# Kernel optimization log

Hardware: AMD Instinct MI355X
Metric: run time of the kernel (lower is better)

Reference implementation:

```python
import jax, jax.numpy as jnp
import numpy as np

L, P = 16384, 512
DT_MIN, DT_MAX = 0.001, 0.1
THRESHOLD = 1.0  # spike threshold assumed for cartesian_spike


def setup_inputs() -> dict:
    key = jax.random.key(0)
    k1, k2, k3, k4, k5, k6 = jax.random.split(key, 6)
    u = jax.random.normal(k1, (L, P), dtype=jnp.float32)
    # Stored Lambda param: [..., 0] = log(-Re(Lambda)) with Re(Lambda) < 0, [..., 1] = Im(Lambda)
    lam_real_neg = jax.random.uniform(k2, (P,), minval=0.1, maxval=1.0)  # -Re(Lambda)
    lam_imag = jax.random.normal(k3, (P,)) * 3.0
    Lambda = jnp.stack([jnp.log(lam_real_neg), lam_imag], axis=-1).astype(jnp.float32)
    # init_log_steps: log(dt) uniform in [log(dt_min), log(dt_max)], shape (P, 1)
    log_step = (np.log(DT_MIN) + jax.random.uniform(k4, (P, 1)) * (np.log(DT_MAX) - np.log(DT_MIN))).astype(jnp.float32)
    V_re = jax.random.normal(k5, (P, P), dtype=jnp.float32) / np.sqrt(P)
    V_im = jax.random.normal(k6, (P, P), dtype=jnp.float32) / np.sqrt(P)
    return {"u": u, "Lambda": Lambda, "log_step": log_step, "V_re": V_re, "V_im": V_im}


def _binop(q_i, q_j):
    A_i, b_i = q_i
    A_j, b_j = q_j
    return (A_j * A_i, A_j * b_i + b_j)


def reference(u, Lambda, log_step, V_re, V_im):
    # keep_imag = False: u stays real. discretization = 'zoh', activation = 'cartesian_spike'.
    Lambda_tilde = -jnp.exp(Lambda[..., 0]) + 1j * Lambda[..., 1]            # (P,) complex
    step = jnp.exp(log_step[:, 0])                                            # (P,)
    Lambda_bar = jnp.exp(Lambda_tilde * step)                                 # (P,) |.|<1
    # B_tilde = I, so zoh gives B_bar = diag((Lambda_bar - 1)/Lambda); B_bar @ u_t = coef * u_t
    B_coef = (Lambda_bar - 1.0) / Lambda_tilde                                # (P,)
    Lambda_elements = jnp.broadcast_to(Lambda_bar, (u.shape[0], Lambda_bar.shape[0]))
    Bu_elements = B_coef[None, :] * u.astype(Lambda_bar.dtype)                # (L, P) complex
    _, xs = jax.lax.associative_scan(_binop, (Lambda_elements, Bu_elements))  # (L, P)
    V = V_re + 1j * V_im
    xs = xs @ V.T                                                             # vmap(V @ x) over L
    spikes = (xs.real > THRESHOLD).astype(jnp.float32)                        # cartesian_spike
    return spikes
```

## Files before the change

kernel.cpp:

```cpp
#include <hip/hip_runtime.h>

#define L_LEN   16384
#define P_DIM   512
#define CHUNK   128
#define NCHUNK  128

#define KDIM    1024
#define NDIM    512
#define BM      128
#define BN      128
#define BK      64

typedef __bf16 bf16_t;
typedef __bf16 bf16x8 __attribute__((ext_vector_type(8)));
typedef float  floatx4 __attribute__((ext_vector_type(4)));

__device__ __forceinline__ void channel_consts(const float* __restrict__ Lam,
                                               const float* __restrict__ lstep,
                                               int p, float& ar, float& ai,
                                               float& br, float& bi) {
    float lr = -expf(Lam[2 * p + 0]);
    float li = Lam[2 * p + 1];
    float s  = expf(lstep[p]);
    float er = expf(lr * s);
    ar = er * cosf(li * s);
    ai = er * sinf(li * s);
    float dr = ar - 1.0f, di = ai;
    float inv = 1.0f / (lr * lr + li * li);
    br = (dr * lr + di * li) * inv;
    bi = (di * lr - dr * li) * inv;
}

__global__ void __launch_bounds__(P_DIM) k_scan_ends(const float* __restrict__ u,
        const float* __restrict__ Lam, const float* __restrict__ lstep,
        float2* __restrict__ endv) {
    int p = threadIdx.x;
    int c = blockIdx.x;
    float ar, ai, br, bi;
    channel_consts(Lam, lstep, p, ar, ai, br, bi);
    float xr = 0.f, xi = 0.f;
    const float* up = u + (size_t)c * CHUNK * P_DIM + p;
    #pragma unroll 8
    for (int k = 0; k < CHUNK; ++k) {
        float uv = up[(size_t)k * P_DIM];
        float nr = ar * xr - ai * xi + br * uv;
        float ni = ar * xi + ai * xr + bi * uv;
        xr = nr; xi = ni;
    }
    endv[c * P_DIM + p] = make_float2(xr, xi);
}

__global__ void __launch_bounds__(P_DIM) k_carry(const float* __restrict__ Lam,
        const float* __restrict__ lstep, const float2* __restrict__ endv,
        float2* __restrict__ carry) {
    int p = threadIdx.x;
    float lr = -expf(Lam[2 * p + 0]);
    float li = Lam[2 * p + 1];
    float s  = expf(lstep[p]);
    float t  = s * (float)CHUNK;
    float er = expf(lr * t);
    float Ar = er * cosf(li * t);
    float Ai = er * sinf(li * t);
    float xr = 0.f, xi = 0.f;
    #pragma unroll 4
    for (int c = 0; c < NCHUNK; ++c) {
        carry[c * P_DIM + p] = make_float2(xr, xi);
        float2 e = endv[c * P_DIM + p];
        float nr = Ar * xr - Ai * xi + e.x;
        float ni = Ar * xi + Ai * xr + e.y;
        xr = nr; xi = ni;
    }
}

__global__ void __launch_bounds__(P_DIM) k_materialize(const float* __restrict__ u,
        const float* __restrict__ Lam, const float* __restrict__ lstep,
        const float2* __restrict__ carry, bf16_t* __restrict__ A) {
    int p = threadIdx.x;
    int c = blockIdx.x;
    float ar, ai, br, bi;
    channel_consts(Lam, lstep, p, ar, ai, br, bi);
    float2 x0 = carry[c * P_DIM + p];
    float xr = x0.x, xi = x0.y;
    const float* up = u + (size_t)c * CHUNK * P_DIM + p;
    bf16_t* Ap = A + (size_t)c * CHUNK * KDIM;
    #pragma unroll 4
    for (int k = 0; k < CHUNK; ++k) {
        float uv = up[(size_t)k * P_DIM];
        float nr = ar * xr - ai * xi + br * uv;
        float ni = ar * xi + ai * xr + bi * uv;
        xr = nr; xi = ni;
        Ap[(size_t)k * KDIM + p]         = (bf16_t)xr;
        Ap[(size_t)k * KDIM + P_DIM + p] = (bf16_t)xi;
    }
}

__global__ void __launch_bounds__(256) k_bt(const float* __restrict__ Vre,
        const float* __restrict__ Vim, bf16_t* __restrict__ Bt) {
    int idx = blockIdx.x * 256 + threadIdx.x;
    int j = idx >> 10;
    int k = idx & 1023;
    float v = (k < P_DIM) ? Vre[j * P_DIM + k] : -Vim[j * P_DIM + (k - P_DIM)];
    Bt[idx] = (bf16_t)v;
}

__global__ void __launch_bounds__(256) k_gemm(const bf16_t* __restrict__ A,
        const bf16_t* __restrict__ Bt, float* __restrict__ out) {
    __shared__ uint4 As4[BM * BK * 2 / 16];
    __shared__ uint4 Bs4[BN * BK * 2 / 16];

    const int tid  = threadIdx.x;
    const int lane = tid & 63;
    const int w    = tid >> 6;
    const int m0   = blockIdx.x * BM;
    const int n0   = blockIdx.y * BN;
    const int wm   = (w >> 1) * 64;
    const int wn   = (w & 1) * 64;

    const int fr_m = lane & 15;
    const int fr_g = lane >> 4;

    floatx4 acc[4][4];
    #pragma unroll
    for (int i = 0; i < 4; ++i)
        #pragma unroll
        for (int j = 0; j < 4; ++j) {
            floatx4 z = {0.f, 0.f, 0.f, 0.f};
            acc[i][j] = z;
        }

    const bf16_t* Asrc = A  + (size_t)m0 * KDIM;
    const bf16_t* Bsrc = Bt + (size_t)n0 * KDIM;

    for (int kt = 0; kt < KDIM; kt += BK) {
        __syncthreads();
        #pragma unroll
        for (int i = 0; i < 4; ++i) {
            int q   = i * 256 + tid;
            int row = q >> 3;
            int sc  = q & 7;
            int gc  = sc ^ (row & 7);
            As4[q] = *((const uint4*)(Asrc + (size_t)row * KDIM + kt) + gc);
            Bs4[q] = *((const uint4*)(Bsrc + (size_t)row * KDIM + kt) + gc);
        }
        __syncthreads();
        #pragma unroll
        for (int kk = 0; kk < BK; kk += 32) {
            bf16x8 af[4], bf[4];
            #pragma unroll
            for (int i = 0; i < 4; ++i) {
                int m  = wm + i * 16 + fr_m;
                int cc = (kk >> 3) + fr_g;
                int sc = cc ^ (m & 7);
                af[i] = *(const bf16x8*)((const bf16_t*)As4 + m * BK + sc * 8);
            }
            #pragma unroll
            for (int j = 0; j < 4; ++j) {
                int n  = wn + j * 16 + fr_m;
                int cc = (kk >> 3) + fr_g;
                int sc = cc ^ (n & 7);
                bf[j] = *(const bf16x8*)((const bf16_t*)Bs4 + n * BK + sc * 8);
            }
            #pragma unroll
            for (int i = 0; i < 4; ++i)
                #pragma unroll
                for (int j = 0; j < 4; ++j)
                    acc[i][j] = __builtin_amdgcn_mfma_f32_16x16x32_bf16(
                        af[i], bf[j], acc[i][j], 0, 0, 0);
        }
    }

    #pragma unroll
    for (int i = 0; i < 4; ++i)
        #pragma unroll
        for (int j = 0; j < 4; ++j)
            #pragma unroll
            for (int r = 0; r < 4; ++r) {
                int rr = wm + i * 16 + fr_g * 4 + r;
                int cl = wn + j * 16 + fr_m;
                float v = acc[i][j][r];
                out[(size_t)(m0 + rr) * NDIM + (n0 + cl)] = (v > 1.0f) ? 1.0f : 0.0f;
            }
}

extern "C" void kernel_launch(void* const* d_in, const int* in_sizes, int n_in,
                              void* d_out, int out_size, void* d_ws, size_t ws_size,
                              hipStream_t stream) {
    (void)in_sizes; (void)n_in; (void)out_size; (void)ws_size;
    const float* u     = (const float*)d_in[0];
    const float* Lam   = (const float*)d_in[1];
    const float* lstep = (const float*)d_in[2];
    const float* Vre   = (const float*)d_in[3];
    const float* Vim   = (const float*)d_in[4];
    float* out = (float*)d_out;

    char* ws = (char*)d_ws;
    const size_t endv_bytes  = (size_t)NCHUNK * P_DIM * sizeof(float2);
    const size_t carry_bytes = endv_bytes;
    const size_t bt_bytes    = (size_t)NDIM * KDIM * sizeof(bf16_t);
    float2* endv  = (float2*)(ws);
    float2* carry = (float2*)(ws + endv_bytes);
    bf16_t* Bt    = (bf16_t*)(ws + endv_bytes + carry_bytes);
    bf16_t* A     = (bf16_t*)(ws + endv_bytes + carry_bytes + bt_bytes);

    hipLaunchKernelGGL(k_scan_ends, dim3(NCHUNK), dim3(P_DIM), 0, stream,
                       u, Lam, lstep, endv);
    hipLaunchKernelGGL(k_bt, dim3(NDIM * KDIM / 256), dim3(256), 0, stream,
                       Vre, Vim, Bt);
    hipLaunchKernelGGL(k_carry, dim3(1), dim3(P_DIM), 0, stream,
                       Lam, lstep, endv, carry);
    hipLaunchKernelGGL(k_materialize, dim3(NCHUNK), dim3(P_DIM), 0, stream,
                       u, Lam, lstep, carry, A);
    hipLaunchKernelGGL(k_gemm, dim3(L_LEN / BM, NDIM / BN), dim3(256), 0, stream,
                       A, Bt, out);
}
```

Measured before the change: 154.8 us.

## Parallelize chunk carry scan, interleave complex K layout, use direct global-to-LDS loads

The serial single-block carry recurrence becomes a log-step parallel scan in shared memory. Each block handles 4 channels by 256 chunks, and the chunk size is halved to 64 so twice as many chunks run. The real and imaginary parts are now interleaved along K in both the activation matrix and the transformed V, which allows packed 32-bit stores. The GEMM tile loads switch to global_load_lds with precomputed pointers. Together these aim to remove the serial carry bottleneck and cut store and load-instruction overhead. The costs are more scan sync steps and reliance on global_load_lds address semantics.

```diff
diff --git a/kernel.cpp b/kernel.cpp
--- a/kernel.cpp
+++ b/kernel.cpp
@@ -2,8 +2,8 @@
 
 #define L_LEN   16384
 #define P_DIM   512
-#define CHUNK   128
-#define NCHUNK  128
+#define CHUNK   64
+#define NCHUNK  256
 
 #define KDIM    1024
 #define NDIM    512
@@ -47,13 +47,19 @@
         float ni = ar * xi + ai * xr + bi * uv;
         xr = nr; xi = ni;
     }
-    endv[c * P_DIM + p] = make_float2(xr, xi);
-}
-
-__global__ void __launch_bounds__(P_DIM) k_carry(const float* __restrict__ Lam,
+    endv[(size_t)c * P_DIM + p] = make_float2(xr, xi);
+}
+
+__global__ void __launch_bounds__(1024) k_carry(const float* __restrict__ Lam,
         const float* __restrict__ lstep, const float2* __restrict__ endv,
         float2* __restrict__ carry) {
-    int p = threadIdx.x;
+    __shared__ float2 zl[4 * (NCHUNK + 2)];
+    int tid = threadIdx.x;
+    int g = tid & 3;
+    int c = tid >> 2;
+    int p = blockIdx.x * 4 + g;
+    int zi_base = g * (NCHUNK + 2);
+
     float lr = -expf(Lam[2 * p + 0]);
     float li = Lam[2 * p + 1];
     float s  = expf(lstep[p]);
@@ -61,15 +67,26 @@
     float er = expf(lr * t);
     float Ar = er * cosf(li * t);
     float Ai = er * sinf(li * t);
-    float xr = 0.f, xi = 0.f;
-    #pragma unroll 4
-    for (int c = 0; c < NCHUNK; ++c) {
-        carry[c * P_DIM + p] = make_float2(xr, xi);
-        float2 e = endv[c * P_DIM + p];
-        float nr = Ar * xr - Ai * xi + e.x;
-        float ni = Ar * xi + Ai * xr + e.y;
-        xr = nr; xi = ni;
-    }
+
+    float2 e = endv[(size_t)c * P_DIM + p];
+    float zr = e.x, zi = e.y;
+    zl[zi_base + c] = make_float2(zr, zi);
+    __syncthreads();
+    for (int st = 1; st < NCHUNK; st <<= 1) {
+        float tr = 0.f, ti = 0.f;
+        if (c >= st) { float2 v = zl[zi_base + c - st]; tr = v.x; ti = v.y; }
+        __syncthreads();
+        zr += Ar * tr - Ai * ti;
+        zi += Ar * ti + Ai * tr;
+        zl[zi_base + c] = make_float2(zr, zi);
+        float nAr = Ar * Ar - Ai * Ai;
+        float nAi = 2.f * Ar * Ai;
+        Ar = nAr; Ai = nAi;
+        __syncthreads();
+    }
+    float2 cv = make_float2(0.f, 0.f);
+    if (c > 0) cv = zl[zi_base + c - 1];
+    carry[(size_t)c * P_DIM + p] = cv;
 }
 
 __global__ void __launch_bounds__(P_DIM) k_materialize(const float* __restrict__ u,
@@ -79,28 +96,31 @@
     int c = blockIdx.x;
     float ar, ai, br, bi;
     channel_consts(Lam, lstep, p, ar, ai, br, bi);
-    float2 x0 = carry[c * P_DIM + p];
+    float2 x0 = carry[(size_t)c * P_DIM + p];
     float xr = x0.x, xi = x0.y;
     const float* up = u + (size_t)c * CHUNK * P_DIM + p;
-    bf16_t* Ap = A + (size_t)c * CHUNK * KDIM;
+    uint32_t* Ap = (uint32_t*)(A + (size_t)c * CHUNK * KDIM) + p;
     #pragma unroll 4
     for (int k = 0; k < CHUNK; ++k) {
         float uv = up[(size_t)k * P_DIM];
         float nr = ar * xr - ai * xi + br * uv;
         float ni = ar * xi + ai * xr + bi * uv;
         xr = nr; xi = ni;
-        Ap[(size_t)k * KDIM + p]         = (bf16_t)xr;
-        Ap[(size_t)k * KDIM + P_DIM + p] = (bf16_t)xi;
+        bf16_t hr = (bf16_t)xr, hi = (bf16_t)xi;
+        uint32_t pk = (uint32_t)__builtin_bit_cast(unsigned short, hr)
+                    | ((uint32_t)__builtin_bit_cast(unsigned short, hi) << 16);
+        Ap[(size_t)k * (KDIM / 2)] = pk;
     }
 }
 
 __global__ void __launch_bounds__(256) k_bt(const float* __restrict__ Vre,
         const float* __restrict__ Vim, bf16_t* __restrict__ Bt) {
     int idx = blockIdx.x * 256 + threadIdx.x;
-    int j = idx >> 10;
-    int k = idx & 1023;
-    float v = (k < P_DIM) ? Vre[j * P_DIM + k] : -Vim[j * P_DIM + (k - P_DIM)];
-    Bt[idx] = (bf16_t)v;
+    bf16_t r = (bf16_t)Vre[idx];
+    bf16_t m = (bf16_t)(-Vim[idx]);
+    uint32_t pk = (uint32_t)__builtin_bit_cast(unsigned short, r)
+                | ((uint32_t)__builtin_bit_cast(unsigned short, m) << 16);
+    ((uint32_t*)Bt)[idx] = pk;
 }
 
 __global__ void __launch_bounds__(256) k_gemm(const bf16_t* __restrict__ A,
@@ -131,16 +151,29 @@
     const bf16_t* Asrc = A  + (size_t)m0 * KDIM;
     const bf16_t* Bsrc = Bt + (size_t)n0 * KDIM;
 
+    const bf16_t* ga[4]; const bf16_t* gb[4];
+    char* la[4]; char* lb[4];
+    #pragma unroll
+    for (int i = 0; i < 4; ++i) {
+        int q   = i * 256 + tid;
+        int row = q >> 3;
+        int gc  = (q & 7) ^ (row & 7);
+        ga[i] = Asrc + (size_t)row * KDIM + gc * 8;
+        gb[i] = Bsrc + (size_t)row * KDIM + gc * 8;
+        la[i] = (char*)As4 + (size_t)q * 16;
+        lb[i] = (char*)Bs4 + (size_t)q * 16;
+    }
+
     for (int kt = 0; kt < KDIM; kt += BK) {
         __syncthreads();
         #pragma unroll
         for (int i = 0; i < 4; ++i) {
-            int q   = i * 256 + tid;
-            int row = q >> 3;
-            int sc  = q & 7;
-            int gc  = sc ^ (row & 7);
-            As4[q] = *((const uint4*)(Asrc + (size_t)row * KDIM + kt) + gc);
-            Bs4[q] = *((const uint4*)(Bsrc + (size_t)row * KDIM + kt) + gc);
+            __builtin_amdgcn_global_load_lds(
+                (const __attribute__((address_space(1))) void*)(ga[i] + kt),
+                (__attribute__((address_space(3))) void*)la[i], 16, 0, 0);
+            __builtin_amdgcn_global_load_lds(
+                (const __attribute__((address_space(1))) void*)(gb[i] + kt),
+                (__attribute__((address_space(3))) void*)lb[i], 16, 0, 0);
         }
         __syncthreads();
         #pragma unroll
@@ -204,9 +237,9 @@
 
     hipLaunchKernelGGL(k_scan_ends, dim3(NCHUNK), dim3(P_DIM), 0, stream,
                        u, Lam, lstep, endv);
-    hipLaunchKernelGGL(k_bt, dim3(NDIM * KDIM / 256), dim3(256), 0, stream,
+    hipLaunchKernelGGL(k_bt, dim3(NDIM * P_DIM / 256), dim3(256), 0, stream,
                        Vre, Vim, Bt);
-    hipLaunchKernelGGL(k_carry, dim3(1), dim3(P_DIM), 0, stream,
+    hipLaunchKernelGGL(k_carry, dim3(P_DIM / 4), dim3(1024), 0, stream,
                        Lam, lstep, endv, carry);
     hipLaunchKernelGGL(k_materialize, dim3(NCHUNK), dim3(P_DIM), 0, stream,
                        u, Lam, lstep, carry, A);
```

After: 128.4 us. -17.0%, faster.
